# Kernel optimization log

Measured on AMD Instinct MI355X. Metric: run time of the kernel, lower is better.

The kernel has to match this reference:

```python
import jax, jax.numpy as jnp
import numpy as np

F_DIM = 256; H = 4; LAT = 256; BOT = 128
B = 64; NPG = 180; N = B * NPG; E = N * 16; HF = H * F_DIM
NEG_SLOPE = 0.2  # PyG GATConv default LeakyReLU slope


def _gat(x, src, dst, W, att_s, att_d, bias):
    # PyG GATConv (concat=True): h = x W, per-edge score LeakyReLU(a_s[src]+a_d[dst]),
    # softmax over incoming edges of each dst, weighted sum, concat heads, + bias.
    h = (x @ W).reshape(N, H, F_DIM)
    a_s = jnp.einsum('nhc,hc->nh', h, att_s)
    a_d = jnp.einsum('nhc,hc->nh', h, att_d)
    e = jax.nn.leaky_relu(a_s[src] + a_d[dst], NEG_SLOPE)          # [E+N, H]
    m = jax.ops.segment_max(e, dst, num_segments=N)                # stable softmax per dst
    p = jnp.exp(e - m[dst])
    s = jax.ops.segment_sum(p, dst, num_segments=N)
    alpha = p / (s[dst] + 1e-16)
    out = jax.ops.segment_sum(alpha[:, :, None] * h[src], dst, num_segments=N)
    return out.reshape(N, HF) + bias


def setup_inputs() -> dict:
    key = jax.random.key(0)
    ks = jax.random.split(key, 40)
    def rn(i, shape, scale):
        return jax.random.normal(ks[i], shape, jnp.float32) * jnp.float32(scale)
    inp = {}
    inp['z'] = jax.random.normal(ks[0], (B, LAT), jnp.float32)
    inp['condition'] = jax.random.normal(ks[1], (B, BOT), jnp.float32)
    dst = jax.random.randint(ks[2], (E,), 0, N)
    off = jax.random.randint(ks[3], (E,), 1, NPG)
    src = (dst + off) % N  # no self-loops by construction (PyG adds them itself)
    inp['edge_index'] = jnp.stack([src, dst]).astype(jnp.int32)
    inp['batch'] = jnp.repeat(jnp.arange(B, dtype=jnp.int32), NPG)
    def lin(i, fin, fout):
        s = 1.0 / np.sqrt(fin)
        return rn(i, (fin, fout), s), rn(i + 1, (fout,), s)
    inp['W_init'], inp['b_init'] = lin(4, LAT + BOT, F_DIM)
    inp['W1'] = rn(6, (F_DIM + 180, HF), 1.0 / np.sqrt(F_DIM + 180))
    inp['as1'] = rn(7, (H, F_DIM), 0.1); inp['ad1'] = rn(8, (H, F_DIM), 0.1)
    inp['b1'] = rn(9, (HF,), 0.1)
    inp['W2'] = rn(10, (HF, HF), 1.0 / np.sqrt(HF))
    inp['as2'] = rn(11, (H, F_DIM), 0.1); inp['ad2'] = rn(12, (H, F_DIM), 0.1)
    inp['b2'] = rn(13, (HF,), 0.1)
    inp['W3'] = rn(14, (HF, HF), 1.0 / np.sqrt(HF))
    inp['as3'] = rn(15, (H, F_DIM), 0.1); inp['ad3'] = rn(16, (H, F_DIM), 0.1)
    inp['b3'] = rn(17, (HF,), 0.1)
    inp['Wp'], inp['bp'] = lin(18, HF, F_DIM)
    inp['Wfp'], inp['bfp'] = lin(20, F_DIM, 2)
    inp['Ws'], inp['bs'] = lin(22, HF, F_DIM)
    inp['Wfs'], inp['bfs'] = lin(24, F_DIM, 2)
    inp['Wt'], inp['bt'] = lin(26, HF, F_DIM)
    inp['Wft'], inp['bft'] = lin(28, F_DIM, 1)
    return inp


def reference(z, condition, edge_index, batch, W_init, b_init,
              W1, as1, ad1, b1, W2, as2, ad2, b2, W3, as3, ad3, b3,
              Wp, bp, Wfp, bfp, Ws, bs, Wfs, bfs, Wt, bt, Wft, bft):
    zc = jnp.concatenate([z, condition], axis=1) @ W_init + b_init  # [B, F]
    x = zc[batch]                                                    # [N, F]
    # node order within each (sorted) batch segment -> one-hot(180)
    start = jnp.searchsorted(batch, jnp.arange(B, dtype=batch.dtype))
    order = jnp.arange(N) - start[batch]
    pos = jax.nn.one_hot(order, 180, dtype=x.dtype)
    x = jax.nn.relu(jnp.concatenate([x, pos], axis=1))               # [N, F+180]
    # add self loops (PyG GATConv default add_self_loops=True)
    loops = jnp.arange(N, dtype=edge_index.dtype)
    src = jnp.concatenate([edge_index[0], loops])
    dst = jnp.concatenate([edge_index[1], loops])
    x = jax.nn.relu(_gat(x, src, dst, W1, as1, ad1, b1))
    x = jax.nn.relu(_gat(x, src, dst, W2, as2, ad2, b2))
    x = jax.nn.relu(_gat(x, src, dst, W3, as3, ad3, b3))
    out_pos = jax.nn.relu(x @ Wp + bp) @ Wfp + bfp     # [N, 2]
    out_size = jax.nn.relu(x @ Ws + bs) @ Wfs + bfs    # [N, 2]
    out_theta = jax.nn.relu(x @ Wt + bt) @ Wft + bft   # [N, 1]
    return out_pos, out_size, out_theta
```

## Files before the change

kernel.cpp:

```cpp
#include <hip/hip_runtime.h>
#include <hip/hip_bf16.h>

#define NODES 11520
#define EDGES 184320
#define NB    64
#define NPG   180
#define CAP   64

typedef __bf16 bf16x8 __attribute__((ext_vector_type(8)));
typedef __bf16 bf16x4 __attribute__((ext_vector_type(4)));
typedef float  f32x4  __attribute__((ext_vector_type(4)));

__global__ __launch_bounds__(256) void k_init(
    const float* __restrict__ z, const float* __restrict__ cond,
    const float* __restrict__ Wi, const float* __restrict__ bi,
    const float* __restrict__ W1, float* __restrict__ Y1)
{
    __shared__ float xr[384];
    __shared__ float part[4][256];
    __shared__ float zr[256];
    const int b = blockIdx.x, t = threadIdx.x;
    xr[t] = (t < 256) ? z[b * 256 + t] : 0.f;
    if (t < 128) xr[256 + t] = cond[b * 128 + t];
    __syncthreads();
    {
        const int kq = t >> 6, tc = t & 63;
        f32x4 acc = {0.f, 0.f, 0.f, 0.f};
        const float* wbase = Wi + (size_t)(kq * 96) * 256 + 4 * tc;
        const float* xb = xr + kq * 96;
#pragma unroll 8
        for (int k = 0; k < 96; ++k) {
            const float4 w = *(const float4*)(wbase + (size_t)k * 256);
            const float x = xb[k];
            acc[0] = fmaf(x, w.x, acc[0]);
            acc[1] = fmaf(x, w.y, acc[1]);
            acc[2] = fmaf(x, w.z, acc[2]);
            acc[3] = fmaf(x, w.w, acc[3]);
        }
        *(f32x4*)&part[kq][4 * tc] = acc;
    }
    __syncthreads();
    zr[t] = fmaxf(bi[t] + part[0][t] + part[1][t] + part[2][t] + part[3][t], 0.f);
    __syncthreads();
    {
        f32x4 acc = {0.f, 0.f, 0.f, 0.f};
#pragma unroll 8
        for (int k = 0; k < 256; ++k) {
            const float4 w = *(const float4*)(W1 + (size_t)k * 1024 + 4 * t);
            const float x = zr[k];
            acc[0] = fmaf(x, w.x, acc[0]);
            acc[1] = fmaf(x, w.y, acc[1]);
            acc[2] = fmaf(x, w.z, acc[2]);
            acc[3] = fmaf(x, w.w, acc[3]);
        }
        *(f32x4*)(Y1 + (size_t)b * 1024 + 4 * t) = acc;
    }
}

__global__ __launch_bounds__(256) void k_h1(
    const float* __restrict__ Y1, const float* __restrict__ W1,
    const float* __restrict__ atts, const float* __restrict__ attd,
    __bf16* __restrict__ hb, float* __restrict__ asb, float* __restrict__ adb,
    float* __restrict__ zas, float* __restrict__ zad)
{
    const int n = blockIdx.x, t = threadIdx.x;
    if (t < 4)      zas[n * 4 + t] = 0.f;
    else if (t < 8) zad[n * 4 + (t - 4)] = 0.f;
    const int g = n / NPG, o = n - g * NPG;
    const float4 y = *(const float4*)(Y1 + (size_t)g * 1024 + 4 * t);
    const float4 w = *(const float4*)(W1 + (size_t)(256 + o) * 1024 + 4 * t);
    const float4 h = {y.x + w.x, y.y + w.y, y.z + w.z, y.w + w.w};
    bf16x4 hv = {(__bf16)h.x, (__bf16)h.y, (__bf16)h.z, (__bf16)h.w};
    *(bf16x4*)(hb + (size_t)n * 1024 + 4 * t) = hv;
    const int head = t >> 6, c0 = (t & 63) * 4;
    const float4 s4 = *(const float4*)(atts + head * 256 + c0);
    const float4 d4 = *(const float4*)(attd + head * 256 + c0);
    float ps = h.x * s4.x + h.y * s4.y + h.z * s4.z + h.w * s4.w;
    float pd = h.x * d4.x + h.y * d4.y + h.z * d4.z + h.w * d4.w;
    for (int off = 32; off; off >>= 1) {
        ps += __shfl_xor(ps, off, 64);
        pd += __shfl_xor(pd, off, 64);
    }
    if ((t & 63) == 0) { asb[n * 4 + head] = ps; adb[n * 4 + head] = pd; }
}

__global__ __launch_bounds__(256) void k_hist(
    const int* __restrict__ ei, int* __restrict__ counts,
    int* __restrict__ bucket)
{
    const int e = blockIdx.x * 256 + threadIdx.x;
    if (e >= EDGES) return;
    const int s = ei[e], d = ei[EDGES + e];
    const int pos = atomicAdd(&counts[d], 1);
    if (pos < CAP) bucket[(size_t)d * CAP + pos] = s;
}

__global__ __launch_bounds__(256) void k_agg(
    const __bf16* __restrict__ hb, const float* __restrict__ asb,
    const float* __restrict__ adb, const int* __restrict__ counts,
    const int* __restrict__ bucket, const float* __restrict__ bias,
    __bf16* __restrict__ xout, float* __restrict__ zas, float* __restrict__ zad)
{
    const int b = blockIdx.x;
    const int nb = (b & 7) * (NODES / 8) + 2 * (b >> 3);
    const int t = threadIdx.x;
    const int half = t >> 7, tt = t & 127;
    const int n = nb + half;
    __shared__ float sc[2][CAP + 1][4];
    __shared__ int   ssrc[2][CAP + 1];
    __shared__ float sinv[2][4];
    if (zas != nullptr) {
        if (t < 8)       zas[nb * 4 + t] = 0.f;
        else if (t < 16) zad[nb * 4 + (t - 8)] = 0.f;
    }
    const int deg = min(counts[n], CAP);
    const int ne  = deg + 1;
    if (tt < deg)       ssrc[half][tt] = bucket[(size_t)n * CAP + tt];
    else if (tt == deg) ssrc[half][tt] = n;
    __syncthreads();
    if (tt < ne) {
        const int s = ssrc[half][tt];
        const float4 as4 = *(const float4*)(asb + (size_t)s * 4);
        const float4 ad4 = *(const float4*)(adb + (size_t)n * 4);
        const float v0 = as4.x + ad4.x, v1 = as4.y + ad4.y;
        const float v2 = as4.z + ad4.z, v3 = as4.w + ad4.w;
        sc[half][tt][0] = v0 > 0.f ? v0 : 0.2f * v0;
        sc[half][tt][1] = v1 > 0.f ? v1 : 0.2f * v1;
        sc[half][tt][2] = v2 > 0.f ? v2 : 0.2f * v2;
        sc[half][tt][3] = v3 > 0.f ? v3 : 0.2f * v3;
    }
    __syncthreads();
    const int ln = t & 63, hw = (t >> 6) & 1;
#pragma unroll
    for (int hh = 0; hh < 2; ++hh) {
        const int head = hw * 2 + hh;
        float m = -1e30f;
        for (int k = ln; k < ne; k += 64) m = fmaxf(m, sc[half][k][head]);
        for (int off = 32; off; off >>= 1) m = fmaxf(m, __shfl_xor(m, off, 64));
        float s = 0.f;
        for (int k = ln; k < ne; k += 64) {
            const float p = __expf(sc[half][k][head] - m);
            sc[half][k][head] = p;
            s += p;
        }
        for (int off = 32; off; off >>= 1) s += __shfl_xor(s, off, 64);
        if (ln == 0) sinv[half][head] = 1.f / (s + 1e-16f);
    }
    __syncthreads();
    const int j0 = tt * 8, hd = tt >> 5;
    const float inv = sinv[half][hd];
    float a[8] = {0, 0, 0, 0, 0, 0, 0, 0};
    int k = 0;
    for (; k + 4 <= ne; k += 4) {
        float al[4]; bf16x8 hv[4];
#pragma unroll
        for (int u = 0; u < 4; ++u) {
            al[u] = sc[half][k + u][hd] * inv;
            hv[u] = *(const bf16x8*)(hb + (size_t)ssrc[half][k + u] * 1024 + j0);
        }
#pragma unroll
        for (int u = 0; u < 4; ++u)
#pragma unroll
            for (int e = 0; e < 8; ++e)
                a[e] = fmaf(al[u], (float)hv[u][e], a[e]);
    }
    for (; k < ne; ++k) {
        const float al = sc[half][k][hd] * inv;
        const bf16x8 hv = *(const bf16x8*)(hb + (size_t)ssrc[half][k] * 1024 + j0);
#pragma unroll
        for (int e = 0; e < 8; ++e)
            a[e] = fmaf(al, (float)hv[e], a[e]);
    }
    const float4 b4a = *(const float4*)(bias + j0);
    const float4 b4b = *(const float4*)(bias + j0 + 4);
    bf16x8 o;
    o[0] = (__bf16)fmaxf(a[0] + b4a.x, 0.f);
    o[1] = (__bf16)fmaxf(a[1] + b4a.y, 0.f);
    o[2] = (__bf16)fmaxf(a[2] + b4a.z, 0.f);
    o[3] = (__bf16)fmaxf(a[3] + b4a.w, 0.f);
    o[4] = (__bf16)fmaxf(a[4] + b4b.x, 0.f);
    o[5] = (__bf16)fmaxf(a[5] + b4b.y, 0.f);
    o[6] = (__bf16)fmaxf(a[6] + b4b.z, 0.f);
    o[7] = (__bf16)fmaxf(a[7] + b4b.w, 0.f);
    *(bf16x8*)(xout + (size_t)n * 1024 + j0) = o;
}

__global__ __launch_bounds__(256) void k_transW(
    const float* __restrict__ W2, const float* __restrict__ W3,
    __bf16* __restrict__ W2t, __bf16* __restrict__ W3t)
{
    const float* W = blockIdx.z ? W3 : W2;
    __bf16* WT = blockIdx.z ? W3t : W2t;
    __shared__ float t[32][33];
    const int n0 = blockIdx.x * 32, k0 = blockIdx.y * 32;
    const int tx = threadIdx.x & 31, ty = threadIdx.x >> 5;
#pragma unroll
    for (int i = 0; i < 32; i += 8)
        t[ty + i][tx] = W[(size_t)(k0 + ty + i) * 1024 + n0 + tx];
    __syncthreads();
#pragma unroll
    for (int i = 0; i < 32; i += 8)
        WT[(size_t)(n0 + ty + i) * 1024 + k0 + tx] = (__bf16)t[tx][ty + i];
}

__global__ __launch_bounds__(256) void k_transH(
    const float* __restrict__ Wp, const float* __restrict__ Ws,
    const float* __restrict__ Wt, __bf16* __restrict__ WHt,
    const float* __restrict__ bp, const float* __restrict__ bs,
    const float* __restrict__ bt, float* __restrict__ bc)
{
    if (blockIdx.x == 8) {
        if (blockIdx.y == 0) {
            const int t = blockIdx.z * 256 + threadIdx.x;
            const float v = blockIdx.z == 0 ? bp[threadIdx.x]
                          : blockIdx.z == 1 ? bs[threadIdx.x] : bt[threadIdx.x];
            bc[t] = v;
        }
        return;
    }
    const float* W = blockIdx.z == 0 ? Wp : blockIdx.z == 1 ? Ws : Wt;
    __bf16* WT = WHt + (size_t)blockIdx.z * 256 * 1024;
    __shared__ float t[32][33];
    const int n0 = blockIdx.x * 32, k0 = blockIdx.y * 32;
    const int tx = threadIdx.x & 31, ty = threadIdx.x >> 5;
#pragma unroll
    for (int i = 0; i < 32; i += 8)
        t[ty + i][tx] = W[(size_t)(k0 + ty + i) * 256 + n0 + tx];
    __syncthreads();
#pragma unroll
    for (int i = 0; i < 32; i += 8)
        WT[(size_t)(n0 + ty + i) * 1024 + k0 + tx] = (__bf16)t[tx][ty + i];
}

#define STAGE(buf, kbase)                                                      \
    {                                                                          \
        _Pragma("unroll")                                                      \
        for (int h = 0; h < 2; ++h) {                                          \
            _Pragma("unroll")                                                  \
            for (int cc = 0; cc < 2; ++cc) {                                   \
                const int c = 2 * w + cc;                                      \
                const int row = c * 16 + lr;                                   \
                __builtin_amdgcn_global_load_lds(                              \
                    (const __attribute__((address_space(1))) void*)            \
                        (A + (size_t)(m0 + row) * K + (kbase) + h * 32 + lk),  \
                    (__attribute__((address_space(3))) void*)                  \
                        (As + (buf) * 8192 + h * 4096 + c * 512), 16, 0, 0);   \
                __builtin_amdgcn_global_load_lds(                              \
                    (const __attribute__((address_space(1))) void*)            \
                        (BT + (size_t)(n0 + row) * K + (kbase) + h * 32 + lk), \
                    (__attribute__((address_space(3))) void*)                  \
                        (Bs + (buf) * 8192 + h * 4096 + c * 512), 16, 0, 0);   \
            }                                                                  \
        }                                                                      \
    }

#define COMPUTE(buf)                                                           \
    {                                                                          \
        _Pragma("unroll")                                                      \
        for (int h = 0; h < 2; ++h) {                                          \
            bf16x8 af[4], bfr[4];                                              \
            _Pragma("unroll")                                                  \
            for (int i = 0; i < 4; ++i)                                        \
                af[i] = *(const bf16x8*)(As + (buf) * 8192 + h * 4096 +        \
                                         (wm + i * 16 + r16) * 32 + quad * 8); \
            _Pragma("unroll")                                                  \
            for (int j = 0; j < 4; ++j)                                        \
                bfr[j] = *(const bf16x8*)(Bs + (buf) * 8192 + h * 4096 +       \
                                          (wn + j * 16 + r16) * 32 + quad * 8);\
            _Pragma("unroll")                                                  \
            for (int i = 0; i < 4; ++i)                                        \
                _Pragma("unroll")                                              \
                for (int j = 0; j < 4; ++j)                                    \
                    acc[i][j] = __builtin_amdgcn_mfma_f32_16x16x32_bf16(       \
                        af[i], bfr[j], acc[i][j], 0, 0, 0);                    \
        }                                                                      \
    }

#define GEMM_MAINLOOP()                                                        \
    f32x4 acc[4][4];                                                           \
    _Pragma("unroll")                                                          \
    for (int i = 0; i < 4; ++i)                                                \
        _Pragma("unroll")                                                      \
        for (int j = 0; j < 4; ++j)                                            \
            acc[i][j] = (f32x4){0.f, 0.f, 0.f, 0.f};                           \
    STAGE(0, 0);                                                               \
    int cur = 0;                                                               \
    for (int k0 = 64; k0 < K; k0 += 64) {                                      \
        __syncthreads();                                                       \
        STAGE(cur ^ 1, k0);                                                    \
        COMPUTE(cur);                                                          \
        cur ^= 1;                                                              \
    }                                                                          \
    __syncthreads();                                                           \
    COMPUTE(cur);

__global__ __launch_bounds__(256) void gemm_bf16_h(
    const __bf16* __restrict__ A, const __bf16* __restrict__ BT,
    __bf16* __restrict__ Cb,
    const float* __restrict__ atts, const float* __restrict__ attd,
    float* __restrict__ asb, float* __restrict__ adb,
    int M, int N, int K)
{
    const int lb = blockIdx.x;
    const int g = lb & 7, idx = lb >> 3;
    const int bx = idx & 7;
    const int by = (idx >> 3) * 8 + g;
    if (by * 128 >= M) return;
    const int m0 = by * 128, n0 = bx * 128;

    __shared__ __bf16 As[2 * 128 * 64];
    __shared__ __bf16 Bs[2 * 128 * 64];
    const int tid = threadIdx.x;
    const int w = tid >> 6, l = tid & 63;
    const int lr = l >> 2, lk = (l & 3) * 8;
    const int quad = l >> 4, r16 = l & 15;
    const int wm = (w >> 1) * 64, wn = (w & 1) * 64;

    GEMM_MAINLOOP();

    const int head = (n0 + wn) >> 8;
    float sa[4], da[4];
#pragma unroll
    for (int j = 0; j < 4; ++j) {
        const int cl = (n0 + wn + j * 16 + r16) & 255;
        sa[j] = atts[head * 256 + cl];
        da[j] = attd[head * 256 + cl];
    }
#pragma unroll
    for (int i = 0; i < 4; ++i) {
#pragma unroll
        for (int r = 0; r < 4; ++r) {
            const int mg = m0 + wm + i * 16 + quad * 4 + r;
            float ps = 0.f, pd = 0.f;
#pragma unroll
            for (int j = 0; j < 4; ++j) {
                const int ng = n0 + wn + j * 16 + r16;
                const float v = acc[i][j][r];
                ps = fmaf(v, sa[j], ps);
                pd = fmaf(v, da[j], pd);
                Cb[(size_t)mg * N + ng] = (__bf16)v;
            }
            for (int off = 8; off; off >>= 1) {
                ps += __shfl_xor(ps, off, 64);
                pd += __shfl_xor(pd, off, 64);
            }
            if (r16 == 0) {
                atomicAdd(&asb[mg * 4 + head], ps);
                atomicAdd(&adb[mg * 4 + head], pd);
            }
        }
    }
}

__global__ __launch_bounds__(256) void gemm_heads(
    const __bf16* __restrict__ A, const __bf16* __restrict__ BT,
    const float* __restrict__ biascat,
    const float* __restrict__ Wfp, const float* __restrict__ bfp,
    const float* __restrict__ Wfs, const float* __restrict__ bfs,
    const float* __restrict__ Wft, const float* __restrict__ bft,
    float* __restrict__ out, int M, int K)
{
    const int lb = blockIdx.x;
    const int g = lb & 7, idx = lb >> 3;
    const int bx = idx % 6;
    const int by = (idx / 6) * 8 + g;
    if (by * 128 >= M) return;
    const int m0 = by * 128, n0 = bx * 128;

    __shared__ __bf16 As[2 * 128 * 64];
    __shared__ __bf16 Bs[2 * 128 * 64];
    const int tid = threadIdx.x;
    const int w = tid >> 6, l = tid & 63;
    const int lr = l >> 2, lk = (l & 3) * 8;
    const int quad = l >> 4, r16 = l & 15;
    const int wm = (w >> 1) * 64, wn = (w & 1) * 64;

    GEMM_MAINLOOP();

    const int hg = bx >> 1;
    const float* Wf = hg == 0 ? Wfp : hg == 1 ? Wfs : Wft;
    const int nout = hg == 2 ? 1 : 2;
    float wf0[4], wf1[4], bz[4];
#pragma unroll
    for (int j = 0; j < 4; ++j) {
        const int ng = n0 + wn + j * 16 + r16;
        const int cl = ng & 255;
        bz[j]  = biascat[ng];
        wf0[j] = Wf[cl * nout];
        wf1[j] = nout == 2 ? Wf[cl * nout + 1] : 0.f;
    }
    const bool addb = ((bx & 1) == 0) && (wn == 0);
    const float fb0 = hg == 0 ? bfp[0] : hg == 1 ? bfs[0] : bft[0];
    const float fb1 = hg == 2 ? 0.f : (hg == 0 ? bfp[1] : bfs[1]);
#pragma unroll
    for (int i = 0; i < 4; ++i) {
#pragma unroll
        for (int r = 0; r < 4; ++r) {
            const int mg = m0 + wm + i * 16 + quad * 4 + r;
            float o0 = 0.f, o1 = 0.f;
#pragma unroll
            for (int j = 0; j < 4; ++j) {
                const float v = fmaxf(acc[i][j][r] + bz[j], 0.f);
                o0 = fmaf(v, wf0[j], o0);
                o1 = fmaf(v, wf1[j], o1);
            }
            for (int off = 8; off; off >>= 1) {
                o0 += __shfl_xor(o0, off, 64);
                o1 += __shfl_xor(o1, off, 64);
            }
            if (r16 == 0) {
                if (addb) { o0 += fb0; o1 += fb1; }
                const size_t base = hg == 0 ? 2 * (size_t)mg
                                 : hg == 1 ? 2 * (size_t)NODES + 2 * (size_t)mg
                                 : 4 * (size_t)NODES + (size_t)mg;
                atomicAdd(&out[base], o0);
                if (nout == 2) atomicAdd(&out[base + 1], o1);
            }
        }
    }
}

extern "C" void kernel_launch(void* const* d_in, const int* in_sizes, int n_in,
                              void* d_out, int out_size, void* d_ws, size_t ws_size,
                              hipStream_t stream)
{
    const float* z    = (const float*)d_in[0];
    const float* cond = (const float*)d_in[1];
    const int*   ei   = (const int*)  d_in[2];
    const float* Wi   = (const float*)d_in[4];
    const float* bi   = (const float*)d_in[5];
    const float* W1   = (const float*)d_in[6];
    const float* as1  = (const float*)d_in[7];
    const float* ad1  = (const float*)d_in[8];
    const float* b1   = (const float*)d_in[9];
    const float* W2   = (const float*)d_in[10];
    const float* as2  = (const float*)d_in[11];
    const float* ad2  = (const float*)d_in[12];
    const float* b2   = (const float*)d_in[13];
    const float* W3   = (const float*)d_in[14];
    const float* as3  = (const float*)d_in[15];
    const float* ad3  = (const float*)d_in[16];
    const float* b3   = (const float*)d_in[17];
    const float* Wp   = (const float*)d_in[18];
    const float* bp   = (const float*)d_in[19];
    const float* Wfp  = (const float*)d_in[20];
    const float* bfp  = (const float*)d_in[21];
    const float* Ws   = (const float*)d_in[22];
    const float* bs   = (const float*)d_in[23];
    const float* Wfs  = (const float*)d_in[24];
    const float* bfs  = (const float*)d_in[25];
    const float* Wt   = (const float*)d_in[26];
    const float* bt   = (const float*)d_in[27];
    const float* Wft  = (const float*)d_in[28];
    const float* bft  = (const float*)d_in[29];
    float* out = (float*)d_out;

    char* p = (char*)d_ws;
    __bf16* hb    = (__bf16*)p;           p += (size_t)NODES * 1024 * 2;
    __bf16* xb16  = (__bf16*)p;           p += (size_t)NODES * 1024 * 2;
    float* asA    = (float*)p;            p += (size_t)NODES * 4 * 4;
    float* adA    = (float*)p;            p += (size_t)NODES * 4 * 4;
    float* asB    = (float*)p;            p += (size_t)NODES * 4 * 4;
    float* adB    = (float*)p;            p += (size_t)NODES * 4 * 4;
    float* Y1     = (float*)p;            p += 64 * 1024 * 4;
    int*   counts = (int*)p;              p += (size_t)NODES * 4;
    int*   bucket = (int*)p;              p += (size_t)NODES * CAP * 4;
    __bf16* W2t   = (__bf16*)p;           p += (size_t)1024 * 1024 * 2;
    __bf16* W3t   = (__bf16*)p;           p += (size_t)1024 * 1024 * 2;
    __bf16* WHt   = (__bf16*)p;           p += (size_t)768 * 1024 * 2;
    float* biascat= (float*)p;            p += 768 * 4;

    hipMemsetAsync(out, 0, (size_t)out_size * sizeof(float), stream);
    hipMemsetAsync(counts, 0, NODES * sizeof(int), stream);

    k_transW<<<dim3(32, 32, 2), 256, 0, stream>>>(W2, W3, W2t, W3t);
    k_transH<<<dim3(9, 32, 3), 256, 0, stream>>>(Wp, Ws, Wt, WHt,
                                                 bp, bs, bt, biascat);
    k_hist<<<EDGES / 256, 256, 0, stream>>>(ei, counts, bucket);

    k_init<<<NB, 256, 0, stream>>>(z, cond, Wi, bi, W1, Y1);
    k_h1<<<NODES, 256, 0, stream>>>(Y1, W1, as1, ad1, hb, asA, adA, asB, adB);
    k_agg<<<NODES / 2, 256, 0, stream>>>(hb, asA, adA, counts, bucket, b1,
                                         xb16, nullptr, nullptr);

    gemm_bf16_h<<<8 * 96, 256, 0, stream>>>(xb16, W2t, hb, as2, ad2,
                                            asB, adB, NODES, 1024, 1024);
    k_agg<<<NODES / 2, 256, 0, stream>>>(hb, asB, adB, counts, bucket, b2,
                                         xb16, asA, adA);
    gemm_bf16_h<<<8 * 96, 256, 0, stream>>>(xb16, W3t, hb, as3, ad3,
                                            asA, adA, NODES, 1024, 1024);
    k_agg<<<NODES / 2, 256, 0, stream>>>(hb, asA, adA, counts, bucket, b3,
                                         xb16, nullptr, nullptr);

    gemm_heads<<<6 * 96, 256, 0, stream>>>(xb16, WHt, biascat,
                                           Wfp, bfp, Wfs, bfs, Wft, bft,
                                           out, NODES, 1024);
}
```

Measured before the change: 431.8 us.

## Load GEMM fragments directly from global memory into registers, dropping LDS staging

Replaces the LDS double-buffered staging (global_load_lds plus barriers) in both GEMM kernels with per-wave register double-buffering: each wave loads its MFMA A/B fragments straight from global memory and alternates two fragment sets across 32-wide k steps. This removes the __syncthreads and the LDS read traffic, and frees the shared-memory allocation, which may raise occupancy. In exchange, data that the block used to share through LDS is now fetched separately by each wave (A rows by two waves, B rows by two waves), which raises global/L2 traffic. The 16-byte row-strided loads are also less coalesced than before.

```diff
diff --git a/kernel.cpp b/kernel.cpp
--- a/kernel.cpp
+++ b/kernel.cpp
@@ -232,48 +232,23 @@
         WT[(size_t)(n0 + ty + i) * 1024 + k0 + tx] = (__bf16)t[tx][ty + i];
 }
 
-#define STAGE(buf, kbase)                                                      \
+#define LOAD_FRAGS(aa, bb, kk)                                                 \
     {                                                                          \
         _Pragma("unroll")                                                      \
-        for (int h = 0; h < 2; ++h) {                                          \
-            _Pragma("unroll")                                                  \
-            for (int cc = 0; cc < 2; ++cc) {                                   \
-                const int c = 2 * w + cc;                                      \
-                const int row = c * 16 + lr;                                   \
-                __builtin_amdgcn_global_load_lds(                              \
-                    (const __attribute__((address_space(1))) void*)            \
-                        (A + (size_t)(m0 + row) * K + (kbase) + h * 32 + lk),  \
-                    (__attribute__((address_space(3))) void*)                  \
-                        (As + (buf) * 8192 + h * 4096 + c * 512), 16, 0, 0);   \
-                __builtin_amdgcn_global_load_lds(                              \
-                    (const __attribute__((address_space(1))) void*)            \
-                        (BT + (size_t)(n0 + row) * K + (kbase) + h * 32 + lk), \
-                    (__attribute__((address_space(3))) void*)                  \
-                        (Bs + (buf) * 8192 + h * 4096 + c * 512), 16, 0, 0);   \
-            }                                                                  \
+        for (int i = 0; i < 4; ++i) {                                          \
+            aa[i] = *(const bf16x8*)(Ab + (size_t)i * 16 * K + (kk));          \
+            bb[i] = *(const bf16x8*)(Bb + (size_t)i * 16 * K + (kk));          \
         }                                                                      \
     }
 
-#define COMPUTE(buf)                                                           \
+#define MFMA_TILE(aa, bb)                                                      \
     {                                                                          \
         _Pragma("unroll")                                                      \
-        for (int h = 0; h < 2; ++h) {                                          \
-            bf16x8 af[4], bfr[4];                                              \
-            _Pragma("unroll")                                                  \
-            for (int i = 0; i < 4; ++i)                                        \
-                af[i] = *(const bf16x8*)(As + (buf) * 8192 + h * 4096 +        \
-                                         (wm + i * 16 + r16) * 32 + quad * 8); \
+        for (int i = 0; i < 4; ++i)                                            \
             _Pragma("unroll")                                                  \
             for (int j = 0; j < 4; ++j)                                        \
-                bfr[j] = *(const bf16x8*)(Bs + (buf) * 8192 + h * 4096 +       \
-                                          (wn + j * 16 + r16) * 32 + quad * 8);\
-            _Pragma("unroll")                                                  \
-            for (int i = 0; i < 4; ++i)                                        \
-                _Pragma("unroll")                                              \
-                for (int j = 0; j < 4; ++j)                                    \
-                    acc[i][j] = __builtin_amdgcn_mfma_f32_16x16x32_bf16(       \
-                        af[i], bfr[j], acc[i][j], 0, 0, 0);                    \
-        }                                                                      \
+                acc[i][j] = __builtin_amdgcn_mfma_f32_16x16x32_bf16(           \
+                    aa[i], bb[j], acc[i][j], 0, 0, 0);                         \
     }
 
 #define GEMM_MAINLOOP()                                                        \
@@ -283,16 +258,17 @@
         _Pragma("unroll")                                                      \
         for (int j = 0; j < 4; ++j)                                            \
             acc[i][j] = (f32x4){0.f, 0.f, 0.f, 0.f};                           \
-    STAGE(0, 0);                                                               \
-    int cur = 0;                                                               \
+    bf16x8 a0[4], b0[4], a1[4], b1[4];                                         \
+    LOAD_FRAGS(a0, b0, 0);                                                     \
+    LOAD_FRAGS(a1, b1, 32);                                                    \
     for (int k0 = 64; k0 < K; k0 += 64) {                                      \
-        __syncthreads();                                                       \
-        STAGE(cur ^ 1, k0);                                                    \
-        COMPUTE(cur);                                                          \
-        cur ^= 1;                                                              \
+        MFMA_TILE(a0, b0);                                                     \
+        LOAD_FRAGS(a0, b0, k0);                                                \
+        MFMA_TILE(a1, b1);                                                     \
+        LOAD_FRAGS(a1, b1, k0 + 32);                                           \
     }                                                                          \
-    __syncthreads();                                                           \
-    COMPUTE(cur);
+    MFMA_TILE(a0, b0);                                                         \
+    MFMA_TILE(a1, b1);
 
 __global__ __launch_bounds__(256) void gemm_bf16_h(
     const __bf16* __restrict__ A, const __bf16* __restrict__ BT,
@@ -308,13 +284,13 @@
     if (by * 128 >= M) return;
     const int m0 = by * 128, n0 = bx * 128;
 
-    __shared__ __bf16 As[2 * 128 * 64];
-    __shared__ __bf16 Bs[2 * 128 * 64];
     const int tid = threadIdx.x;
     const int w = tid >> 6, l = tid & 63;
-    const int lr = l >> 2, lk = (l & 3) * 8;
     const int quad = l >> 4, r16 = l & 15;
     const int wm = (w >> 1) * 64, wn = (w & 1) * 64;
+
+    const __bf16* Ab = A  + (size_t)(m0 + wm + r16) * K + quad * 8;
+    const __bf16* Bb = BT + (size_t)(n0 + wn + r16) * K + quad * 8;
 
     GEMM_MAINLOOP();
 
@@ -367,13 +343,13 @@
     if (by * 128 >= M) return;
     const int m0 = by * 128, n0 = bx * 128;
 
-    __shared__ __bf16 As[2 * 128 * 64];
-    __shared__ __bf16 Bs[2 * 128 * 64];
     const int tid = threadIdx.x;
     const int w = tid >> 6, l = tid & 63;
-    const int lr = l >> 2, lk = (l & 3) * 8;
     const int quad = l >> 4, r16 = l & 15;
     const int wm = (w >> 1) * 64, wn = (w & 1) * 64;
+
+    const __bf16* Ab = A  + (size_t)(m0 + wm + r16) * K + quad * 8;
+    const __bf16* Bb = BT + (size_t)(n0 + wn + r16) * K + quad * 8;
 
     GEMM_MAINLOOP();
 
```

Measured after the change: 532.2 us. +23.3%, slower.
